# Optimization experiments

Measured on AMD Instinct MI355X. Metric: run time of the kernel, lower is better.

The kernel has to match this reference:

```python
import jax, jax.numpy as jnp
import numpy as np

B, S, H, NH = 2, 2048, 1024, 16
HD = H // NH  # 64
SCALE = HD ** -0.5


def setup_inputs() -> dict:
    key = jax.random.key(0)
    k1, k2, k3 = jax.random.split(key, 3)
    x = jax.random.normal(k1, (B, S, H), dtype=jnp.float32)
    w_qkv = jax.random.normal(k2, (H, 3 * H), dtype=jnp.float32) * (H ** -0.5)
    b_qkv = jnp.zeros((3 * H,), dtype=jnp.float32)
    w_out = jax.random.normal(k3, (H, H), dtype=jnp.float32) * (H ** -0.5)
    b_out = jnp.zeros((H,), dtype=jnp.float32)
    return {"x": x, "w_qkv": w_qkv, "b_qkv": b_qkv, "w_out": w_out, "b_out": b_out}


def reference(x, w_qkv, b_qkv, w_out, b_out):
    # qkv projection: [B,S,3H] -> split -> [B,NH,S,HD] each
    qkv = x @ w_qkv + b_qkv
    q, k, v = jnp.split(qkv, 3, axis=-1)
    def heads(t):
        return t.reshape(B, S, NH, HD).transpose(0, 2, 1, 3)  # [B,NH,S,HD]
    q, k, v = heads(q), heads(k), heads(v)
    # full (non-causal) softmax attention; chunking in the original is
    # math-equivalent since each query row attends over all keys
    scores = jnp.einsum('bhqd,bhkd->bhqk', q, k) * SCALE
    attn = jax.nn.softmax(scores, axis=-1)
    out = jnp.einsum('bhqk,bhkd->bhqd', attn, v)  # [B,NH,S,HD]
    out = out.transpose(0, 2, 1, 3).reshape(B, S, H)
    # to_out linear (Dropout is identity in eval mode)
    return out @ w_out + b_out
```

## Files before the change

kernel.cpp:

```cpp
#include <hip/hip_runtime.h>
#include <cstdint>

using u16 = unsigned short;
typedef __bf16 bf16x8 __attribute__((ext_vector_type(8)));
typedef __bf16 bf16x4 __attribute__((ext_vector_type(4)));
typedef __bf16 bf16x2 __attribute__((ext_vector_type(2)));
typedef float f32x4 __attribute__((ext_vector_type(4)));

#define MFMA16(a, b, c) __builtin_amdgcn_mfma_f32_16x16x32_bf16((a), (b), (c), 0, 0, 0)

__device__ __forceinline__ u16 f2bf(float f) {
  union { float f; uint32_t u; } c; c.f = f;
  uint32_t u = c.u;
  u += 0x7fffu + ((u >> 16) & 1u);
  return (u16)(u >> 16);
}

#if __has_builtin(__builtin_amdgcn_global_load_lds)
#define GLOAD_LDS16(g, l)                                                      \
  __builtin_amdgcn_global_load_lds(                                            \
      (__attribute__((address_space(1))) void*)(g),                            \
      (__attribute__((address_space(3))) void*)(l), 16, 0, 0)
#else
#define GLOAD_LDS16(g, l) do { *(uint4*)(l) = *(const uint4*)(g); } while (0)
#endif

__device__ __forceinline__ bf16x8 ptrans(const f32x4 lo, const f32x4 hi) {
  union W { bf16x2 h; uint32_t u; } wl0, wl1, wh0, wh1;
  wl0.h[0] = (__bf16)lo[0]; wl0.h[1] = (__bf16)lo[1];
  wl1.h[0] = (__bf16)lo[2]; wl1.h[1] = (__bf16)lo[3];
  wh0.h[0] = (__bf16)hi[0]; wh0.h[1] = (__bf16)hi[1];
  wh1.h[0] = (__bf16)hi[2]; wh1.h[1] = (__bf16)hi[3];
  uint32_t a0 = wl0.u, b0 = wh0.u, a1 = wl1.u, b1 = wh1.u;
  asm("v_permlane32_swap_b32 %0, %1" : "+v"(a0), "+v"(b0));
  asm("v_permlane16_swap_b32 %0, %1" : "+v"(a0), "+v"(b0));
  asm("v_permlane32_swap_b32 %0, %1" : "+v"(a1), "+v"(b1));
  asm("v_permlane16_swap_b32 %0, %1" : "+v"(a1), "+v"(b1));
  union R { uint32_t u[4]; bf16x8 v; } r;
  r.u[0] = a0; r.u[1] = a1; r.u[2] = b0; r.u[3] = b1;
  return r.v;
}

__global__ __launch_bounds__(256) void prep(
    const float* __restrict__ x, const float* __restrict__ w_qkv,
    const float* __restrict__ w_out, u16* __restrict__ xb,
    u16* __restrict__ wqT, u16* __restrict__ woT) {
  const int bid = blockIdx.x, tid = threadIdx.x;
  if (bid < 4096) {
    int i = (bid * 256 + tid) * 4;
    float4 v = *(const float4*)&x[i];
    ushort4 p;
    p.x = f2bf(v.x); p.y = f2bf(v.y); p.z = f2bf(v.z); p.w = f2bf(v.w);
    *(ushort4*)&xb[i] = p;
    return;
  }
  __shared__ float tile[32][33];
  int t = bid - 4096;
  const float* in;
  u16* outp;
  int C, bx, by;
  if (t < 3072) { in = w_qkv; outp = wqT; C = 3072; bx = (t % 96) * 32; by = (t / 96) * 32; }
  else { t -= 3072; in = w_out; outp = woT; C = 1024; bx = (t % 32) * 32; by = (t / 32) * 32; }
  const int tx = tid & 31, ty = tid >> 5;
#pragma unroll
  for (int r2 = 0; r2 < 4; ++r2)
    tile[ty + r2 * 8][tx] = in[(size_t)(by + ty + r2 * 8) * C + bx + tx];
  __syncthreads();
#pragma unroll
  for (int r2 = 0; r2 < 4; ++r2)
    outp[(size_t)(bx + ty + r2 * 8) * 1024 + by + tx] = f2bf(tile[tx][ty + r2 * 8]);
}

__global__ __launch_bounds__(256, 3) void gemm_qkv(
    const u16* __restrict__ A, const u16* __restrict__ Bt,
    const float* __restrict__ bias,
    u16* __restrict__ qb, u16* __restrict__ kb, u16* __restrict__ vb,
    int M, int N, int K) {
  __shared__ u16 As[128 * 32];
  __shared__ u16 Bs[128 * 32];
  const int tid = threadIdx.x;
  const int m0 = blockIdx.x * 128;
  const int n0 = blockIdx.y * 128;
  const int lane = tid & 63, w = tid >> 6;
  const int quad = lane >> 4, l16 = lane & 15;
  const int wr = w >> 1, wc = w & 1;

  f32x4 acc[4][4] = {};

  const int r0 = tid >> 2, p0 = tid & 3;
  const int r1 = r0 + 64;
  const int c8 = p0 ^ ((r0 >> 1) & 3);
  const u16* ga0 = A + (size_t)(m0 + r0) * K + c8 * 8;
  const u16* ga1 = A + (size_t)(m0 + r1) * K + c8 * 8;
  const u16* gb0 = Bt + (size_t)(n0 + r0) * K + c8 * 8;
  const u16* gb1 = Bt + (size_t)(n0 + r1) * K + c8 * 8;
  u16* la0 = &As[tid * 8];
  u16* la1 = &As[(tid + 256) * 8];
  u16* lb0 = &Bs[tid * 8];
  u16* lb1 = &Bs[(tid + 256) * 8];

  int aoff[4], boff[4];
#pragma unroll
  for (int i = 0; i < 4; ++i) {
    int ra = wr * 64 + i * 16 + l16;
    aoff[i] = (ra * 4 + (quad ^ ((ra >> 1) & 3))) * 8;
    int rb = wc * 64 + i * 16 + l16;
    boff[i] = (rb * 4 + (quad ^ ((rb >> 1) & 3))) * 8;
  }

  const int nIter = K >> 5;
  for (int kt = 0; kt < nIter; ++kt) {
    __syncthreads();
    const int kk = kt << 5;
    GLOAD_LDS16(ga0 + kk, la0);
    GLOAD_LDS16(ga1 + kk, la1);
    GLOAD_LDS16(gb0 + kk, lb0);
    GLOAD_LDS16(gb1 + kk, lb1);
    __syncthreads();
    bf16x8 af[4], bfr[4];
#pragma unroll
    for (int i = 0; i < 4; ++i) af[i] = *(const bf16x8*)&As[aoff[i]];
#pragma unroll
    for (int j = 0; j < 4; ++j) bfr[j] = *(const bf16x8*)&Bs[boff[j]];
#pragma unroll
    for (int i = 0; i < 4; ++i)
#pragma unroll
      for (int j = 0; j < 4; ++j)
        acc[i][j] = MFMA16(af[i], bfr[j], acc[i][j]);
  }

  const int S = 2048, NH = 16;
#pragma unroll
  for (int i = 0; i < 4; ++i) {
    const int mb = m0 + wr * 64 + i * 16 + quad * 4;
#pragma unroll
    for (int j = 0; j < 4; ++j) {
      const int n = n0 + wc * 64 + j * 16 + l16;
      const float bv = bias[n];
      const int which = n >> 10;
      const int hn = n & 1023;
      const int h = hn >> 6, d = hn & 63;
      const int b = mb >> 11, s = mb & 2047;
      const int bh = b * NH + h;
      if (which == 2) {
        ushort4 pk;
        pk.x = f2bf(acc[i][j][0] + bv);
        pk.y = f2bf(acc[i][j][1] + bv);
        pk.z = f2bf(acc[i][j][2] + bv);
        pk.w = f2bf(acc[i][j][3] + bv);
        *(ushort4*)&vb[((size_t)bh * 64 + d) * S + s] = pk;
      } else {
        const float sc = (which == 0) ? 0.18033688f : 1.0f;
        u16* dst = (which == 0) ? qb : kb;
#pragma unroll
        for (int r = 0; r < 4; ++r)
          dst[((size_t)bh * S + s + r) * 64 + d] = f2bf((acc[i][j][r] + bv) * sc);
      }
    }
  }
}

__global__ __launch_bounds__(256, 2) void gemm_out(
    const u16* __restrict__ A, const u16* __restrict__ Bt,
    const float* __restrict__ bias, float* __restrict__ outf,
    int M, int N, int K) {
  __shared__ u16 As[64 * 32];
  __shared__ u16 Bs[128 * 32];
  const int tid = threadIdx.x;
  const int m0 = blockIdx.x * 64;
  const int n0 = blockIdx.y * 128;
  const int lane = tid & 63, w = tid >> 6;
  const int quad = lane >> 4, l16 = lane & 15;
  const int wr = w >> 1, wc = w & 1;

  f32x4 acc[2][4] = {};

  const int r0 = tid >> 2, p0 = tid & 3;
  const int c8 = p0 ^ ((r0 >> 1) & 3);
  const u16* ga0 = A + (size_t)(m0 + r0) * K + c8 * 8;
  const u16* gb0 = Bt + (size_t)(n0 + r0) * K + c8 * 8;
  const u16* gb1 = Bt + (size_t)(n0 + r0 + 64) * K + c8 * 8;
  u16* la0 = &As[tid * 8];
  u16* lb0 = &Bs[tid * 8];
  u16* lb1 = &Bs[(tid + 256) * 8];

  int aoff[2], boff[4];
#pragma unroll
  for (int i = 0; i < 2; ++i) {
    int ra = wr * 32 + i * 16 + l16;
    aoff[i] = (ra * 4 + (quad ^ ((ra >> 1) & 3))) * 8;
  }
#pragma unroll
  for (int j = 0; j < 4; ++j) {
    int rb = wc * 64 + j * 16 + l16;
    boff[j] = (rb * 4 + (quad ^ ((rb >> 1) & 3))) * 8;
  }

  const int nIter = K >> 5;
  for (int kt = 0; kt < nIter; ++kt) {
    __syncthreads();
    const int kk = kt << 5;
    GLOAD_LDS16(ga0 + kk, la0);
    GLOAD_LDS16(gb0 + kk, lb0);
    GLOAD_LDS16(gb1 + kk, lb1);
    __syncthreads();
    bf16x8 af[2], bfr[4];
#pragma unroll
    for (int i = 0; i < 2; ++i) af[i] = *(const bf16x8*)&As[aoff[i]];
#pragma unroll
    for (int j = 0; j < 4; ++j) bfr[j] = *(const bf16x8*)&Bs[boff[j]];
#pragma unroll
    for (int i = 0; i < 2; ++i)
#pragma unroll
      for (int j = 0; j < 4; ++j)
        acc[i][j] = MFMA16(af[i], bfr[j], acc[i][j]);
  }

#pragma unroll
  for (int i = 0; i < 2; ++i) {
    const int mb = m0 + wr * 32 + i * 16 + quad * 4;
#pragma unroll
    for (int j = 0; j < 4; ++j) {
      const int n = n0 + wc * 64 + j * 16 + l16;
      const float bv = bias[n];
#pragma unroll
      for (int r = 0; r < 4; ++r)
        outf[(size_t)(mb + r) * N + n] = acc[i][j][r] + bv;
    }
  }
}

__global__ __launch_bounds__(256, 3) void attn_fa(
    const u16* __restrict__ qg, const u16* __restrict__ kg,
    const u16* __restrict__ vg, u16* __restrict__ o) {
  const int S = 2048;
  const int lin = blockIdx.x;
  const int xcd = lin & 7, chunk = lin >> 3;
  const int bh = xcd * 4 + (chunk & 3);
  const int qblk = chunk >> 2;
  const int b = bh >> 4, h = bh & 15;
  const int tid = threadIdx.x, w = tid >> 6, lane = tid & 63;
  const int quad = lane >> 4, l16 = lane & 15;

  __shared__ u16 Ks[2][8192];

  const int q0 = qblk * 128 + w * 32;
  const u16* qp = qg + ((size_t)bh * S + q0 + l16) * 64 + quad * 8;
  const bf16x8 qf00 = *(const bf16x8*)qp;
  const bf16x8 qf01 = *(const bf16x8*)(qp + 32);
  const bf16x8 qf10 = *(const bf16x8*)(qp + 1024);
  const bf16x8 qf11 = *(const bf16x8*)(qp + 1024 + 32);

  f32x4 accO0[4] = {}, accO1[4] = {};
  f32x4 accL0 = {}, accL1 = {};

  bf16x8 ones;
#pragma unroll
  for (int i = 0; i < 8; ++i) ones[i] = (__bf16)1.0f;

  const u16* kbase = kg + (size_t)bh * S * 64;
  const u16* vbase = vg + (size_t)bh * 64 * S;

  const int sr0 = tid >> 3, sp0 = tid & 7;
  const int c8s = sp0 ^ (sr0 & 7);
  const u16* kSrc = kbase + (size_t)sr0 * 64 + c8s * 8;

  const u16* vB = vbase + (size_t)l16 * S + quad * 8;

  const int kgA = (quad ^ (l16 & 7)) * 8;
  const int kgB = ((quad + 4) ^ (l16 & 7)) * 8;

#pragma unroll
  for (int seg = 0; seg < 4; ++seg)
    GLOAD_LDS16(kSrc + (size_t)seg * 32 * 64, &Ks[0][(seg * 256 + tid) * 8]);

  for (int kt = 0; kt < 16; ++kt) {
    const int cur = kt & 1;
    __syncthreads();
    if (kt + 1 < 16) {
      const int nb = cur ^ 1;
#pragma unroll
      for (int seg = 0; seg < 4; ++seg)
        GLOAD_LDS16(kSrc + (size_t)((kt + 1) * 128 + seg * 32) * 64,
                    &Ks[nb][(seg * 256 + tid) * 8]);
    }
    const u16* Kc = Ks[cur];

#pragma unroll
    for (int hh = 0; hh < 2; ++hh) {
      bf16x8 vl0[4], vl1[4];
      const size_t vcol = (size_t)(kt * 128 + hh * 64);
#pragma unroll
      for (int ct = 0; ct < 4; ++ct) {
        vl0[ct] = *(const bf16x8*)&vB[(size_t)ct * 16 * S + vcol];
        vl1[ct] = *(const bf16x8*)&vB[(size_t)ct * 16 * S + vcol + 32];
      }

      bf16x8 kf0[4], kf1[4];
#pragma unroll
      for (int ct = 0; ct < 4; ++ct) {
        const int rb = (hh * 64 + ct * 16 + l16) * 64;
        kf0[ct] = *(const bf16x8*)&Kc[rb + kgA];
        kf1[ct] = *(const bf16x8*)&Kc[rb + kgB];
      }
      f32x4 s0[4] = {}, s1[4] = {};
      __builtin_amdgcn_s_setprio(1);
#pragma unroll
      for (int ct = 0; ct < 4; ++ct) {
        s0[ct] = MFMA16(kf0[ct], qf00, s0[ct]);
        s0[ct] = MFMA16(kf1[ct], qf01, s0[ct]);
        s1[ct] = MFMA16(kf0[ct], qf10, s1[ct]);
        s1[ct] = MFMA16(kf1[ct], qf11, s1[ct]);
      }
      __builtin_amdgcn_s_setprio(0);

#pragma unroll
      for (int ct = 0; ct < 4; ++ct)
#pragma unroll
        for (int r = 0; r < 4; ++r) {
          s0[ct][r] = __builtin_amdgcn_exp2f(s0[ct][r]);
          s1[ct][r] = __builtin_amdgcn_exp2f(s1[ct][r]);
        }

      bf16x8 pf00 = ptrans(s0[0], s0[1]);
      bf16x8 pf01 = ptrans(s0[2], s0[3]);
      bf16x8 pf10 = ptrans(s1[0], s1[1]);
      bf16x8 pf11 = ptrans(s1[2], s1[3]);

      __builtin_amdgcn_s_setprio(1);
      accL0 = MFMA16(ones, pf00, accL0);
      accL0 = MFMA16(ones, pf01, accL0);
      accL1 = MFMA16(ones, pf10, accL1);
      accL1 = MFMA16(ones, pf11, accL1);

#pragma unroll
      for (int ct = 0; ct < 4; ++ct) {
        accO0[ct] = MFMA16(vl0[ct], pf00, accO0[ct]);
        accO0[ct] = MFMA16(vl1[ct], pf01, accO0[ct]);
        accO1[ct] = MFMA16(vl0[ct], pf10, accO1[ct]);
        accO1[ct] = MFMA16(vl1[ct], pf11, accO1[ct]);
      }
      __builtin_amdgcn_s_setprio(0);
    }
  }

  const float inv0 = 1.f / accL0[0], inv1 = 1.f / accL1[0];

  const int s0r = q0 + l16, s1r = q0 + 16 + l16;
#pragma unroll
  for (int ct = 0; ct < 4; ++ct) {
    ushort4 pk;
    pk.x = f2bf(accO0[ct][0] * inv0);
    pk.y = f2bf(accO0[ct][1] * inv0);
    pk.z = f2bf(accO0[ct][2] * inv0);
    pk.w = f2bf(accO0[ct][3] * inv0);
    *(ushort4*)&o[(size_t)(b * S + s0r) * 1024 + h * 64 + ct * 16 + quad * 4] = pk;
    pk.x = f2bf(accO1[ct][0] * inv1);
    pk.y = f2bf(accO1[ct][1] * inv1);
    pk.z = f2bf(accO1[ct][2] * inv1);
    pk.w = f2bf(accO1[ct][3] * inv1);
    *(ushort4*)&o[(size_t)(b * S + s1r) * 1024 + h * 64 + ct * 16 + quad * 4] = pk;
  }
}


extern "C" void kernel_launch(void* const* d_in, const int* in_sizes, int n_in,
                              void* d_out, int out_size, void* d_ws, size_t ws_size,
                              hipStream_t stream) {
  const float* x = (const float*)d_in[0];
  const float* w_qkv = (const float*)d_in[1];
  const float* b_qkv = (const float*)d_in[2];
  const float* w_out = (const float*)d_in[3];
  const float* b_out = (const float*)d_in[4];
  float* out = (float*)d_out;

  u16* xb = (u16*)d_ws;
  u16* wqT = xb + 4096 * 1024;
  u16* woT = wqT + 3072 * 1024;
  u16* qb = woT + 1024 * 1024;
  u16* kb = qb + 4194304;
  u16* vb = kb + 4194304;
  u16* ao = vb + 4194304;

  prep<<<8192, 256, 0, stream>>>(x, w_qkv, w_out, xb, wqT, woT);
  gemm_qkv<<<dim3(32, 24), 256, 0, stream>>>(xb, wqT, b_qkv, qb, kb, vb,
                                             4096, 3072, 1024);
  attn_fa<<<512, 256, 0, stream>>>(qb, kb, vb, ao);
  gemm_out<<<dim3(64, 8), 256, 0, stream>>>(ao, woT, b_out, out,
                                            4096, 1024, 1024);
}
```

Baseline: 201.6 us.

## Stage V through LDS and software-pipeline QK/softmax with PV across tiles

Attention now stages V tiles into a second double-buffered LDS array alongside K, instead of reading V directly from global memory per wave. The loop is restructured so each iteration computes QK^T and softmax for the current key tile while running the PV MFMAs for the previous tile's probabilities, using ping-pong probability registers. The aim is to hide global-load latency and exp/transpose latency behind MFMA work. In exchange it doubles LDS usage, raises register pressure, adds a second barrier per iteration and lowers launch_bounds occupancy from 3 to 2 blocks.

```diff
diff --git a/kernel.cpp b/kernel.cpp
--- a/kernel.cpp
+++ b/kernel.cpp
@@ -230,7 +230,7 @@
   }
 }
 
-__global__ __launch_bounds__(256, 3) void attn_fa(
+__global__ __launch_bounds__(256, 2) void attn_fa(
     const u16* __restrict__ qg, const u16* __restrict__ kg,
     const u16* __restrict__ vg, u16* __restrict__ o) {
   const int S = 2048;
@@ -243,6 +243,7 @@
   const int quad = lane >> 4, l16 = lane & 15;
 
   __shared__ u16 Ks[2][8192];
+  __shared__ u16 Vs[2][8192];
 
   const int q0 = qblk * 128 + w * 32;
   const u16* qp = qg + ((size_t)bh * S + q0 + l16) * 64 + quad * 8;
@@ -264,84 +265,136 @@
   const int sr0 = tid >> 3, sp0 = tid & 7;
   const int c8s = sp0 ^ (sr0 & 7);
   const u16* kSrc = kbase + (size_t)sr0 * 64 + c8s * 8;
-
-  const u16* vB = vbase + (size_t)l16 * S + quad * 8;
+  const u16* vSrc = vbase + (size_t)sr0 * S + c8s * 8;
 
   const int kgA = (quad ^ (l16 & 7)) * 8;
   const int kgB = ((quad + 4) ^ (l16 & 7)) * 8;
 
-#pragma unroll
-  for (int seg = 0; seg < 4; ++seg)
-    GLOAD_LDS16(kSrc + (size_t)seg * 32 * 64, &Ks[0][(seg * 256 + tid) * 8]);
-
-  for (int kt = 0; kt < 16; ++kt) {
-    const int cur = kt & 1;
-    __syncthreads();
-    if (kt + 1 < 16) {
-      const int nb = cur ^ 1;
-#pragma unroll
-      for (int seg = 0; seg < 4; ++seg)
-        GLOAD_LDS16(kSrc + (size_t)((kt + 1) * 128 + seg * 32) * 64,
-                    &Ks[nb][(seg * 256 + tid) * 8]);
-    }
-    const u16* Kc = Ks[cur];
-
-#pragma unroll
-    for (int hh = 0; hh < 2; ++hh) {
-      bf16x8 vl0[4], vl1[4];
-      const size_t vcol = (size_t)(kt * 128 + hh * 64);
-#pragma unroll
-      for (int ct = 0; ct < 4; ++ct) {
-        vl0[ct] = *(const bf16x8*)&vB[(size_t)ct * 16 * S + vcol];
-        vl1[ct] = *(const bf16x8*)&vB[(size_t)ct * 16 * S + vcol + 32];
-      }
-
-      bf16x8 kf0[4], kf1[4];
-#pragma unroll
-      for (int ct = 0; ct < 4; ++ct) {
-        const int rb = (hh * 64 + ct * 16 + l16) * 64;
-        kf0[ct] = *(const bf16x8*)&Kc[rb + kgA];
-        kf1[ct] = *(const bf16x8*)&Kc[rb + kgB];
-      }
-      f32x4 s0[4] = {}, s1[4] = {};
-      __builtin_amdgcn_s_setprio(1);
-#pragma unroll
-      for (int ct = 0; ct < 4; ++ct) {
-        s0[ct] = MFMA16(kf0[ct], qf00, s0[ct]);
-        s0[ct] = MFMA16(kf1[ct], qf01, s0[ct]);
-        s1[ct] = MFMA16(kf0[ct], qf10, s1[ct]);
-        s1[ct] = MFMA16(kf1[ct], qf11, s1[ct]);
-      }
-      __builtin_amdgcn_s_setprio(0);
-
-#pragma unroll
-      for (int ct = 0; ct < 4; ++ct)
-#pragma unroll
-        for (int r = 0; r < 4; ++r) {
-          s0[ct][r] = __builtin_amdgcn_exp2f(s0[ct][r]);
-          s1[ct][r] = __builtin_amdgcn_exp2f(s1[ct][r]);
-        }
-
-      bf16x8 pf00 = ptrans(s0[0], s0[1]);
-      bf16x8 pf01 = ptrans(s0[2], s0[3]);
-      bf16x8 pf10 = ptrans(s1[0], s1[1]);
-      bf16x8 pf11 = ptrans(s1[2], s1[3]);
-
-      __builtin_amdgcn_s_setprio(1);
-      accL0 = MFMA16(ones, pf00, accL0);
-      accL0 = MFMA16(ones, pf01, accL0);
-      accL1 = MFMA16(ones, pf10, accL1);
-      accL1 = MFMA16(ones, pf11, accL1);
-
-#pragma unroll
-      for (int ct = 0; ct < 4; ++ct) {
-        accO0[ct] = MFMA16(vl0[ct], pf00, accO0[ct]);
-        accO0[ct] = MFMA16(vl1[ct], pf01, accO0[ct]);
-        accO1[ct] = MFMA16(vl0[ct], pf10, accO1[ct]);
-        accO1[ct] = MFMA16(vl1[ct], pf11, accO1[ct]);
-      }
-      __builtin_amdgcn_s_setprio(0);
-    }
+  bf16x8 pfA[8], pfB[8];
+
+#define STAGE_KV(KT, NB)                                                      \
+  {                                                                           \
+    _Pragma("unroll")                                                         \
+    for (int seg = 0; seg < 4; ++seg) {                                       \
+      GLOAD_LDS16(kSrc + (size_t)((KT) * 128 + seg * 32) * 64,                \
+                  &Ks[NB][(seg * 256 + tid) * 8]);                            \
+      GLOAD_LDS16(vSrc + (size_t)(seg & 1) * 32 * S + (KT) * 128 +            \
+                      (seg >> 1) * 64,                                        \
+                  &Vs[NB][(seg * 256 + tid) * 8]);                            \
+    }                                                                         \
+  }
+
+#define QK_BLOCK(KC)                                                          \
+  bf16x8 kf00[4], kf01[4], kf10[4], kf11[4];                                  \
+  _Pragma("unroll")                                                           \
+  for (int ct = 0; ct < 4; ++ct) {                                            \
+    const int rb0 = (ct * 16 + l16) * 64;                                     \
+    const int rb1 = (64 + ct * 16 + l16) * 64;                                \
+    kf00[ct] = *(const bf16x8*)&(KC)[rb0 + kgA];                              \
+    kf01[ct] = *(const bf16x8*)&(KC)[rb0 + kgB];                              \
+    kf10[ct] = *(const bf16x8*)&(KC)[rb1 + kgA];                              \
+    kf11[ct] = *(const bf16x8*)&(KC)[rb1 + kgB];                              \
+  }                                                                           \
+  f32x4 s0[4] = {}, s1[4] = {}, t0[4] = {}, t1[4] = {};                       \
+  __builtin_amdgcn_s_setprio(1);                                              \
+  _Pragma("unroll")                                                           \
+  for (int ct = 0; ct < 4; ++ct) {                                            \
+    s0[ct] = MFMA16(kf00[ct], qf00, s0[ct]);                                  \
+    s0[ct] = MFMA16(kf01[ct], qf01, s0[ct]);                                  \
+    s1[ct] = MFMA16(kf00[ct], qf10, s1[ct]);                                  \
+    s1[ct] = MFMA16(kf01[ct], qf11, s1[ct]);                                  \
+    t0[ct] = MFMA16(kf10[ct], qf00, t0[ct]);                                  \
+    t0[ct] = MFMA16(kf11[ct], qf01, t0[ct]);                                  \
+    t1[ct] = MFMA16(kf10[ct], qf10, t1[ct]);                                  \
+    t1[ct] = MFMA16(kf11[ct], qf11, t1[ct]);                                  \
+  }                                                                           \
+  __builtin_amdgcn_s_setprio(0);
+
+#define SM_BLOCK(PFC)                                                         \
+  _Pragma("unroll")                                                           \
+  for (int ct = 0; ct < 4; ++ct)                                              \
+    _Pragma("unroll")                                                         \
+    for (int r = 0; r < 4; ++r) {                                             \
+      s0[ct][r] = __builtin_amdgcn_exp2f(s0[ct][r]);                          \
+      s1[ct][r] = __builtin_amdgcn_exp2f(s1[ct][r]);                          \
+      t0[ct][r] = __builtin_amdgcn_exp2f(t0[ct][r]);                          \
+      t1[ct][r] = __builtin_amdgcn_exp2f(t1[ct][r]);                          \
+    }                                                                         \
+  PFC[0] = ptrans(s0[0], s0[1]);                                              \
+  PFC[1] = ptrans(s0[2], s0[3]);                                              \
+  PFC[2] = ptrans(s1[0], s1[1]);                                              \
+  PFC[3] = ptrans(s1[2], s1[3]);                                              \
+  PFC[4] = ptrans(t0[0], t0[1]);                                              \
+  PFC[5] = ptrans(t0[2], t0[3]);                                              \
+  PFC[6] = ptrans(t1[0], t1[1]);                                              \
+  PFC[7] = ptrans(t1[2], t1[3]);
+
+#define PV_BLOCK(PFP)                                                         \
+  __builtin_amdgcn_s_setprio(1);                                              \
+  accL0 = MFMA16(ones, PFP[0], accL0);                                        \
+  accL0 = MFMA16(ones, PFP[1], accL0);                                        \
+  accL1 = MFMA16(ones, PFP[2], accL1);                                        \
+  accL1 = MFMA16(ones, PFP[3], accL1);                                        \
+  accL0 = MFMA16(ones, PFP[4], accL0);                                        \
+  accL0 = MFMA16(ones, PFP[5], accL0);                                        \
+  accL1 = MFMA16(ones, PFP[6], accL1);                                        \
+  accL1 = MFMA16(ones, PFP[7], accL1);                                        \
+  _Pragma("unroll")                                                           \
+  for (int ct = 0; ct < 4; ++ct) {                                            \
+    accO0[ct] = MFMA16(vp0[ct], PFP[0], accO0[ct]);                           \
+    accO0[ct] = MFMA16(vp1[ct], PFP[1], accO0[ct]);                           \
+    accO1[ct] = MFMA16(vp0[ct], PFP[2], accO1[ct]);                           \
+    accO1[ct] = MFMA16(vp1[ct], PFP[3], accO1[ct]);                           \
+    accO0[ct] = MFMA16(vp2[ct], PFP[4], accO0[ct]);                           \
+    accO0[ct] = MFMA16(vp3[ct], PFP[5], accO0[ct]);                           \
+    accO1[ct] = MFMA16(vp2[ct], PFP[6], accO1[ct]);                           \
+    accO1[ct] = MFMA16(vp3[ct], PFP[7], accO1[ct]);                           \
+  }                                                                           \
+  __builtin_amdgcn_s_setprio(0);
+
+#define VREAD(VP)                                                             \
+  bf16x8 vp0[4], vp1[4], vp2[4], vp3[4];                                      \
+  _Pragma("unroll")                                                           \
+  for (int ct = 0; ct < 4; ++ct) {                                            \
+    const int rb0 = (ct * 16 + l16) * 64;                                     \
+    vp0[ct] = *(const bf16x8*)&(VP)[rb0 + kgA];                               \
+    vp1[ct] = *(const bf16x8*)&(VP)[rb0 + kgB];                               \
+    vp2[ct] = *(const bf16x8*)&(VP)[4096 + rb0 + kgA];                        \
+    vp3[ct] = *(const bf16x8*)&(VP)[4096 + rb0 + kgB];                        \
+  }
+
+#define ATTN_BODY(KT, CUR, PFP, PFC, PRE)                                     \
+  {                                                                           \
+    __syncthreads();                                                          \
+    const u16* Kc = Ks[CUR];                                                  \
+    const u16* Vp = Vs[(CUR) ^ 1];                                            \
+    VREAD(Vp)                                                                 \
+    QK_BLOCK(Kc)                                                              \
+    __syncthreads();                                                          \
+    if (PRE) STAGE_KV((KT) + 1, (CUR) ^ 1);                                   \
+    PV_BLOCK(PFP)                                                             \
+    SM_BLOCK(PFC)                                                             \
+  }
+
+  STAGE_KV(0, 0);
+  __syncthreads();
+  STAGE_KV(1, 1);
+  {
+    const u16* Kc = Ks[0];
+    QK_BLOCK(Kc)
+    SM_BLOCK(pfA)
+  }
+
+  for (int kt = 1; kt < 15; kt += 2) {
+    ATTN_BODY(kt, 1, pfA, pfB, true);
+    ATTN_BODY(kt + 1, 0, pfB, pfA, true);
+  }
+  ATTN_BODY(15, 1, pfA, pfB, false);
+
+  {
+    const u16* Vp = Vs[1];
+    VREAD(Vp)
+    PV_BLOCK(pfB)
   }
 
   const float inv0 = 1.f / accL0[0], inv1 = 1.f / accL1[0];
@@ -361,6 +414,12 @@
     pk.w = f2bf(accO1[ct][3] * inv1);
     *(ushort4*)&o[(size_t)(b * S + s1r) * 1024 + h * 64 + ct * 16 + quad * 4] = pk;
   }
+#undef ATTN_BODY
+#undef VREAD
+#undef PV_BLOCK
+#undef SM_BLOCK
+#undef QK_BLOCK
+#undef STAGE_KV
 }
 
 
```

Result: faster. 174.3 us (-13.5%).

## Split attention warps over key halves, stage V in LDS, reduce partials

Applied to the files above, without the earlier changes.

Restructures the flash-attention kernel so each pair of warps shares 64 query rows and splits each 128-key tile between them. V is now staged into LDS alongside K with double buffering, instead of being read per-lane from global memory. The two partial O and row-sum accumulators are combined through LDS at the end. This aims for more register-level reuse of K/V fragments per MFMA and coalesced V loads, at the cost of more registers (launch bounds drop to 2 blocks per CU), extra LDS, and a final reduction step.

```diff
diff --git a/kernel.cpp b/kernel.cpp
--- a/kernel.cpp
+++ b/kernel.cpp
@@ -230,7 +230,7 @@
   }
 }
 
-__global__ __launch_bounds__(256, 3) void attn_fa(
+__global__ __launch_bounds__(256, 2) void attn_fa(
     const u16* __restrict__ qg, const u16* __restrict__ kg,
     const u16* __restrict__ vg, u16* __restrict__ o) {
   const int S = 2048;
@@ -241,18 +241,22 @@
   const int b = bh >> 4, h = bh & 15;
   const int tid = threadIdx.x, w = tid >> 6, lane = tid & 63;
   const int quad = lane >> 4, l16 = lane & 15;
+  const int wq = w >> 1, wk = w & 1;
 
   __shared__ u16 Ks[2][8192];
-
-  const int q0 = qblk * 128 + w * 32;
-  const u16* qp = qg + ((size_t)bh * S + q0 + l16) * 64 + quad * 8;
-  const bf16x8 qf00 = *(const bf16x8*)qp;
-  const bf16x8 qf01 = *(const bf16x8*)(qp + 32);
-  const bf16x8 qf10 = *(const bf16x8*)(qp + 1024);
-  const bf16x8 qf11 = *(const bf16x8*)(qp + 1024 + 32);
-
-  f32x4 accO0[4] = {}, accO1[4] = {};
-  f32x4 accL0 = {}, accL1 = {};
+  __shared__ u16 Vs[2][8192];
+
+  const int q0w = qblk * 128 + wq * 64;
+  bf16x8 qf[4][2];
+#pragma unroll
+  for (int qt = 0; qt < 4; ++qt)
+#pragma unroll
+    for (int dh = 0; dh < 2; ++dh)
+      qf[qt][dh] = *(const bf16x8*)(qg + ((size_t)bh * S + q0w + qt * 16 + l16) * 64 +
+                                    dh * 32 + quad * 8);
+
+  f32x4 accO[4][4] = {};
+  f32x4 accL[4] = {};
 
   bf16x8 ones;
 #pragma unroll
@@ -264,102 +268,128 @@
   const int sr0 = tid >> 3, sp0 = tid & 7;
   const int c8s = sp0 ^ (sr0 & 7);
   const u16* kSrc = kbase + (size_t)sr0 * 64 + c8s * 8;
-
-  const u16* vB = vbase + (size_t)l16 * S + quad * 8;
+  const u16* vSrc = vbase + (size_t)sr0 * S + c8s * 8;
 
   const int kgA = (quad ^ (l16 & 7)) * 8;
   const int kgB = ((quad + 4) ^ (l16 & 7)) * 8;
 
-#pragma unroll
-  for (int seg = 0; seg < 4; ++seg)
-    GLOAD_LDS16(kSrc + (size_t)seg * 32 * 64, &Ks[0][(seg * 256 + tid) * 8]);
+#define STAGE_KV(KT, NB)                                                      \
+  {                                                                           \
+    _Pragma("unroll")                                                         \
+    for (int seg = 0; seg < 4; ++seg) {                                       \
+      GLOAD_LDS16(kSrc + (size_t)((KT) * 128 + seg * 32) * 64,                \
+                  &Ks[NB][(seg * 256 + tid) * 8]);                            \
+      GLOAD_LDS16(vSrc + (size_t)(seg & 1) * 32 * S + (KT) * 128 +            \
+                      (seg >> 1) * 64,                                        \
+                  &Vs[NB][(seg * 256 + tid) * 8]);                            \
+    }                                                                         \
+  }
+
+  STAGE_KV(0, 0);
 
   for (int kt = 0; kt < 16; ++kt) {
     const int cur = kt & 1;
     __syncthreads();
-    if (kt + 1 < 16) {
-      const int nb = cur ^ 1;
-#pragma unroll
-      for (int seg = 0; seg < 4; ++seg)
-        GLOAD_LDS16(kSrc + (size_t)((kt + 1) * 128 + seg * 32) * 64,
-                    &Ks[nb][(seg * 256 + tid) * 8]);
-    }
     const u16* Kc = Ks[cur];
-
-#pragma unroll
-    for (int hh = 0; hh < 2; ++hh) {
-      bf16x8 vl0[4], vl1[4];
-      const size_t vcol = (size_t)(kt * 128 + hh * 64);
-#pragma unroll
-      for (int ct = 0; ct < 4; ++ct) {
-        vl0[ct] = *(const bf16x8*)&vB[(size_t)ct * 16 * S + vcol];
-        vl1[ct] = *(const bf16x8*)&vB[(size_t)ct * 16 * S + vcol + 32];
+    const u16* Vc = Vs[cur];
+
+    bf16x8 kf[4][2];
+#pragma unroll
+    for (int ct = 0; ct < 4; ++ct) {
+      const int rb = (wk * 64 + ct * 16 + l16) * 64;
+      kf[ct][0] = *(const bf16x8*)&Kc[rb + kgA];
+      kf[ct][1] = *(const bf16x8*)&Kc[rb + kgB];
+    }
+
+    if (kt + 1 < 16) STAGE_KV(kt + 1, cur ^ 1);
+
+    f32x4 s[4][4] = {};
+    __builtin_amdgcn_s_setprio(1);
+#pragma unroll
+    for (int ct = 0; ct < 4; ++ct)
+#pragma unroll
+      for (int qt = 0; qt < 4; ++qt) {
+        s[ct][qt] = MFMA16(kf[ct][0], qf[qt][0], s[ct][qt]);
+        s[ct][qt] = MFMA16(kf[ct][1], qf[qt][1], s[ct][qt]);
       }
-
-      bf16x8 kf0[4], kf1[4];
-#pragma unroll
-      for (int ct = 0; ct < 4; ++ct) {
-        const int rb = (hh * 64 + ct * 16 + l16) * 64;
-        kf0[ct] = *(const bf16x8*)&Kc[rb + kgA];
-        kf1[ct] = *(const bf16x8*)&Kc[rb + kgB];
+    __builtin_amdgcn_s_setprio(0);
+
+#pragma unroll
+    for (int ct = 0; ct < 4; ++ct)
+#pragma unroll
+      for (int qt = 0; qt < 4; ++qt)
+#pragma unroll
+        for (int r = 0; r < 4; ++r)
+          s[ct][qt][r] = __builtin_amdgcn_exp2f(s[ct][qt][r]);
+
+    bf16x8 pf[2][4];
+#pragma unroll
+    for (int qt = 0; qt < 4; ++qt) {
+      pf[0][qt] = ptrans(s[0][qt], s[1][qt]);
+      pf[1][qt] = ptrans(s[2][qt], s[3][qt]);
+    }
+
+    bf16x8 vf[4][2];
+#pragma unroll
+    for (int dt = 0; dt < 4; ++dt) {
+      const int rb = wk * 4096 + (dt * 16 + l16) * 64;
+      vf[dt][0] = *(const bf16x8*)&Vc[rb + kgA];
+      vf[dt][1] = *(const bf16x8*)&Vc[rb + kgB];
+    }
+
+    __builtin_amdgcn_s_setprio(1);
+#pragma unroll
+    for (int qt = 0; qt < 4; ++qt) {
+      accL[qt] = MFMA16(ones, pf[0][qt], accL[qt]);
+      accL[qt] = MFMA16(ones, pf[1][qt], accL[qt]);
+    }
+#pragma unroll
+    for (int dt = 0; dt < 4; ++dt)
+#pragma unroll
+      for (int qt = 0; qt < 4; ++qt) {
+        accO[dt][qt] = MFMA16(vf[dt][0], pf[0][qt], accO[dt][qt]);
+        accO[dt][qt] = MFMA16(vf[dt][1], pf[1][qt], accO[dt][qt]);
       }
-      f32x4 s0[4] = {}, s1[4] = {};
-      __builtin_amdgcn_s_setprio(1);
-#pragma unroll
-      for (int ct = 0; ct < 4; ++ct) {
-        s0[ct] = MFMA16(kf0[ct], qf00, s0[ct]);
-        s0[ct] = MFMA16(kf1[ct], qf01, s0[ct]);
-        s1[ct] = MFMA16(kf0[ct], qf10, s1[ct]);
-        s1[ct] = MFMA16(kf1[ct], qf11, s1[ct]);
+    __builtin_amdgcn_s_setprio(0);
+  }
+#undef STAGE_KV
+
+  __syncthreads();
+  float* redO = (float*)&Ks[0][0];
+  float* redL = (float*)&Vs[0][0];
+  if (wk == 1) {
+#pragma unroll
+    for (int dt = 0; dt < 4; ++dt)
+#pragma unroll
+      for (int qt = 0; qt < 4; ++qt)
+        *(f32x4*)&redO[((wq * 16 + dt * 4 + qt) << 8) + lane * 4] = accO[dt][qt];
+    if (quad == 0) {
+#pragma unroll
+      for (int qt = 0; qt < 4; ++qt)
+        redL[wq * 64 + qt * 16 + l16] = accL[qt][0];
+    }
+  }
+  __syncthreads();
+  if (wk == 0) {
+#pragma unroll
+    for (int dt = 0; dt < 4; ++dt)
+#pragma unroll
+      for (int qt = 0; qt < 4; ++qt)
+        accO[dt][qt] += *(const f32x4*)&redO[((wq * 16 + dt * 4 + qt) << 8) + lane * 4];
+#pragma unroll
+    for (int qt = 0; qt < 4; ++qt) {
+      const float inv = 1.f / (accL[qt][0] + redL[wq * 64 + qt * 16 + l16]);
+      const int qrow = q0w + qt * 16 + l16;
+#pragma unroll
+      for (int dt = 0; dt < 4; ++dt) {
+        ushort4 pk;
+        pk.x = f2bf(accO[dt][qt][0] * inv);
+        pk.y = f2bf(accO[dt][qt][1] * inv);
+        pk.z = f2bf(accO[dt][qt][2] * inv);
+        pk.w = f2bf(accO[dt][qt][3] * inv);
+        *(ushort4*)&o[(size_t)(b * S + qrow) * 1024 + h * 64 + dt * 16 + quad * 4] = pk;
       }
-      __builtin_amdgcn_s_setprio(0);
-
-#pragma unroll
-      for (int ct = 0; ct < 4; ++ct)
-#pragma unroll
-        for (int r = 0; r < 4; ++r) {
-          s0[ct][r] = __builtin_amdgcn_exp2f(s0[ct][r]);
-          s1[ct][r] = __builtin_amdgcn_exp2f(s1[ct][r]);
-        }
-
-      bf16x8 pf00 = ptrans(s0[0], s0[1]);
-      bf16x8 pf01 = ptrans(s0[2], s0[3]);
-      bf16x8 pf10 = ptrans(s1[0], s1[1]);
-      bf16x8 pf11 = ptrans(s1[2], s1[3]);
-
-      __builtin_amdgcn_s_setprio(1);
-      accL0 = MFMA16(ones, pf00, accL0);
-      accL0 = MFMA16(ones, pf01, accL0);
-      accL1 = MFMA16(ones, pf10, accL1);
-      accL1 = MFMA16(ones, pf11, accL1);
-
-#pragma unroll
-      for (int ct = 0; ct < 4; ++ct) {
-        accO0[ct] = MFMA16(vl0[ct], pf00, accO0[ct]);
-        accO0[ct] = MFMA16(vl1[ct], pf01, accO0[ct]);
-        accO1[ct] = MFMA16(vl0[ct], pf10, accO1[ct]);
-        accO1[ct] = MFMA16(vl1[ct], pf11, accO1[ct]);
-      }
-      __builtin_amdgcn_s_setprio(0);
-    }
-  }
-
-  const float inv0 = 1.f / accL0[0], inv1 = 1.f / accL1[0];
-
-  const int s0r = q0 + l16, s1r = q0 + 16 + l16;
-#pragma unroll
-  for (int ct = 0; ct < 4; ++ct) {
-    ushort4 pk;
-    pk.x = f2bf(accO0[ct][0] * inv0);
-    pk.y = f2bf(accO0[ct][1] * inv0);
-    pk.z = f2bf(accO0[ct][2] * inv0);
-    pk.w = f2bf(accO0[ct][3] * inv0);
-    *(ushort4*)&o[(size_t)(b * S + s0r) * 1024 + h * 64 + ct * 16 + quad * 4] = pk;
-    pk.x = f2bf(accO1[ct][0] * inv1);
-    pk.y = f2bf(accO1[ct][1] * inv1);
-    pk.z = f2bf(accO1[ct][2] * inv1);
-    pk.w = f2bf(accO1[ct][3] * inv1);
-    *(ushort4*)&o[(size_t)(b * S + s1r) * 1024 + h * 64 + ct * 16 + quad * 4] = pk;
+    }
   }
 }
 
```

After: 175.5 us. 1.15x faster.
